# Performance work log

Measured on AMD Instinct MI355X. Metric: run time of the kernel, lower is better.

The kernel has to match this reference:

```python
import jax, jax.numpy as jnp
import numpy as np

SIGMA = 0.5
ALPHA = 1.0  # current_iter = 0 -> cosine annealing returns alpha_max
KSIZE = 5
B, C, H, W, NBOX = 16, 256, 80, 80, 32


def _gaussian_kernel():
    # matches torch: arange(-5//2+1, 5//2+1) = [-2,-1,0,1,2]
    ax = jnp.arange(-(KSIZE // 2), KSIZE // 2 + 1, dtype=jnp.float32)
    xx, yy = jnp.meshgrid(ax, ax, indexing='ij')
    k = jnp.exp(-(xx ** 2 + yy ** 2) / (2.0 * SIGMA ** 2))
    return (k / k.sum())[None, None]  # [1,1,5,5] OIHW


def setup_inputs() -> dict:
    key = jax.random.key(0)
    k1, k2 = jax.random.split(key)
    x = jax.random.normal(k1, (B, C, H, W), dtype=jnp.float32)
    # normalized xywh boxes in [0,1] (code path box.max() <= 1.0)
    boxes = jax.random.uniform(k2, (B, NBOX, 4), dtype=jnp.float32)
    return {"x": x, "boxes": boxes, "kernel": _gaussian_kernel()}


def _attention_map(boxes, height, width):
    # Vectorized rasterization of all boxes at once (torch loops per box).
    xc, yc, bw, bh = boxes[..., 0], boxes[..., 1], boxes[..., 2], boxes[..., 3]
    # int() truncates toward zero -> jnp.trunc; then clamp as in torch code
    x1 = jnp.maximum(0.0, jnp.trunc((xc - bw / 2) * width)).astype(jnp.int32)
    y1 = jnp.maximum(0.0, jnp.trunc((yc - bh / 2) * height)).astype(jnp.int32)
    x2 = jnp.minimum(float(width - 1), jnp.trunc((xc + bw / 2) * width)).astype(jnp.int32)
    y2 = jnp.minimum(float(height - 1), jnp.trunc((yc + bh / 2) * height)).astype(jnp.int32)
    valid = (x2 > x1) & (y2 > y1)  # [B, N]
    rows = jnp.arange(height, dtype=jnp.int32)[None, None, :, None]  # [1,1,H,1]
    cols = jnp.arange(width, dtype=jnp.int32)[None, None, None, :]   # [1,1,1,W]
    inside = ((rows >= y1[:, :, None, None]) & (rows <= y2[:, :, None, None]) &
              (cols >= x1[:, :, None, None]) & (cols <= x2[:, :, None, None]) &
              valid[:, :, None, None])  # [B,N,H,W]
    mask = jnp.any(inside, axis=1).astype(jnp.float32)  # union over boxes -> [B,H,W]
    return mask[:, None]  # [B,1,H,W]


def _smooth(att, kernel):
    pad = KSIZE // 2
    att = jnp.pad(att, ((0, 0), (0, 0), (pad, pad), (pad, pad)), mode='reflect')
    return jax.lax.conv_general_dilated(
        att, kernel, window_strides=(1, 1), padding='VALID',
        dimension_numbers=('NCHW', 'OIHW', 'NCHW'))


def reference(x, boxes, kernel):
    _, _, height, width = x.shape
    att = _attention_map(boxes, height, width)      # [B,1,H,W]
    att = _smooth(att, kernel)                      # gaussian smoothing (sigma>0)
    return x + ALPHA * att * x                      # broadcast over channels
```

## Files before the change

### kernel.cpp

```cpp
#include <hip/hip_runtime.h>


namespace {
constexpr int kB = 16;
constexpr int kC = 256;
constexpr int kH = 80;
constexpr int kW = 80;
constexpr int kNBox = 32;
constexpr float kAlpha = 1.0f;

__device__ __forceinline__ int reflect_idx(int r, int n) {
    return r < 0 ? -r : (r > n - 1 ? 2 * (n - 1) - r : r);
}
}

__global__ __launch_bounds__(320) void ae_fused_kernel(
    const float* __restrict__ x,
    const float* __restrict__ boxes,
    const float* __restrict__ gk,
    float* __restrict__ out)
{
    __shared__ int sx1[kNBox], sy1[kNBox], sx2[kNBox], sy2[kNBox];
    __shared__ float sk[25];
    __shared__ float smask[5][kW];
    __shared__ __attribute__((aligned(16))) float sfac[kW];

    const int b = blockIdx.x / kH;
    const int h = blockIdx.x % kH;
    const int t = threadIdx.x;

    if (t < kNBox) {
        const float* bp = boxes + (size_t)(b * kNBox + t) * 4;
        float xc = bp[0], yc = bp[1], bw = bp[2], bh = bp[3];
        float fx1 = fmaxf(0.0f, truncf((xc - bw * 0.5f) * (float)kW));
        float fy1 = fmaxf(0.0f, truncf((yc - bh * 0.5f) * (float)kH));
        float fx2 = fminf((float)(kW - 1), truncf((xc + bw * 0.5f) * (float)kW));
        float fy2 = fminf((float)(kH - 1), truncf((yc + bh * 0.5f) * (float)kH));
        int ix1 = (int)fx1, iy1 = (int)fy1, ix2 = (int)fx2, iy2 = (int)fy2;
        bool valid = (ix2 > ix1) && (iy2 > iy1);
        sx1[t] = ix1;
        sx2[t] = ix2;
        sy1[t] = valid ? iy1 : 1;
        sy2[t] = valid ? iy2 : 0;
    } else if (t >= 64 && t < 64 + 25) {
        sk[t - 64] = gk[t - 64];
    }
    __syncthreads();

    for (int p = t; p < 5 * kW; p += 320) {
        int i = p / kW, c = p % kW;
        int rr = reflect_idx(h + i - 2, kH);
        float m = 0.0f;
#pragma unroll
        for (int n = 0; n < kNBox; ++n) {
            bool in = (rr >= sy1[n]) && (rr <= sy2[n]) && (c >= sx1[n]) && (c <= sx2[n]);
            m = in ? 1.0f : m;
        }
        smask[i][c] = m;
    }
    __syncthreads();

    if (t < kW) {
        float acc = 0.0f;
#pragma unroll
        for (int i = 0; i < 5; ++i) {
#pragma unroll
            for (int j = 0; j < 5; ++j) {
                int cc = reflect_idx(t + j - 2, kW);
                acc += sk[i * 5 + j] * smask[i][cc];
            }
        }
        sfac[t] = 1.0f + kAlpha * acc;
    }
    __syncthreads();

    const int j = t % 20;
    const int c0 = t / 20;
    const float4 f4 = *reinterpret_cast<const float4*>(&sfac[j * 4]);
    const size_t rowbase = (size_t)b * (kC * kH * kW / 4) + (size_t)h * (kW / 4);
    const float4* x4 = reinterpret_cast<const float4*>(x) + rowbase;
    float4* o4 = reinterpret_cast<float4*>(out) + rowbase;
#pragma unroll
    for (int it = 0; it < kC / 16; ++it) {
        int c = c0 + it * 16;
        size_t off = (size_t)c * (kH * kW / 4) + j;
        float4 v = x4[off];
        v.x *= f4.x;
        v.y *= f4.y;
        v.z *= f4.z;
        v.w *= f4.w;
        o4[off] = v;
    }
}

extern "C" void kernel_launch(void* const* d_in, const int* in_sizes, int n_in,
                              void* d_out, int out_size, void* d_ws, size_t ws_size,
                              hipStream_t stream) {
    const float* x     = (const float*)d_in[0];
    const float* boxes = (const float*)d_in[1];
    const float* gk    = (const float*)d_in[2];
    float* out         = (float*)d_out;

    dim3 grid(kB * kH);
    dim3 block(320);
    ae_fused_kernel<<<grid, block, 0, stream>>>(x, boxes, gk, out);
}
```

Measured before the change: 201.3 us.

## Split into per-batch rasterize kernel and flat streaming multiply kernel

Moves mask rasterization and Gaussian smoothing into a small kernel that runs once per batch and writes a factor map to workspace. A second kernel then streams x with a flat float4 index, multiplying by the precomputed factor, over many more blocks (3200 instead of 1280). This drops the redundant per-row box rasterization and gives the memory-bound pass simpler addressing and more parallelism. The cost is an extra launch, a serial dependency, and a rasterize stage that uses only 16 blocks. If the workspace is too small it falls back to the old fused kernel.

```diff
diff --git a/kernel.cpp b/kernel.cpp
--- a/kernel.cpp
+++ b/kernel.cpp
@@ -8,10 +8,94 @@
 constexpr int kW = 80;
 constexpr int kNBox = 32;
 constexpr float kAlpha = 1.0f;
+constexpr int kHW = kH * kW;
+constexpr int kHW4 = kHW / 4;
+constexpr int kBF4 = kC * kHW4;
+constexpr size_t kWsNeed = (size_t)kB * kHW * sizeof(float);
 
 __device__ __forceinline__ int reflect_idx(int r, int n) {
     return r < 0 ? -r : (r > n - 1 ? 2 * (n - 1) - r : r);
 }
+}
+
+__global__ __launch_bounds__(256) void ae_rasterize_kernel(
+    const float* __restrict__ boxes,
+    const float* __restrict__ gk,
+    float* __restrict__ fac)
+{
+    __shared__ int sx1[kNBox], sy1[kNBox], sx2[kNBox], sy2[kNBox];
+    __shared__ float sk[25];
+    __shared__ float smask[kH][kW];
+
+    const int b = blockIdx.x;
+    const int t = threadIdx.x;
+
+    if (t < kNBox) {
+        const float* bp = boxes + (size_t)(b * kNBox + t) * 4;
+        float xc = bp[0], yc = bp[1], bw = bp[2], bh = bp[3];
+        float fx1 = fmaxf(0.0f, truncf((xc - bw * 0.5f) * (float)kW));
+        float fy1 = fmaxf(0.0f, truncf((yc - bh * 0.5f) * (float)kH));
+        float fx2 = fminf((float)(kW - 1), truncf((xc + bw * 0.5f) * (float)kW));
+        float fy2 = fminf((float)(kH - 1), truncf((yc + bh * 0.5f) * (float)kH));
+        int ix1 = (int)fx1, iy1 = (int)fy1, ix2 = (int)fx2, iy2 = (int)fy2;
+        bool valid = (ix2 > ix1) && (iy2 > iy1);
+        sx1[t] = ix1;
+        sx2[t] = ix2;
+        sy1[t] = valid ? iy1 : 1;
+        sy2[t] = valid ? iy2 : 0;
+    } else if (t >= 64 && t < 64 + 25) {
+        sk[t - 64] = gk[t - 64];
+    }
+    __syncthreads();
+
+    for (int p = t; p < kHW; p += 256) {
+        int h = p / kW, w = p % kW;
+        float m = 0.0f;
+#pragma unroll
+        for (int n = 0; n < kNBox; ++n) {
+            bool in = (h >= sy1[n]) && (h <= sy2[n]) && (w >= sx1[n]) && (w <= sx2[n]);
+            m = in ? 1.0f : m;
+        }
+        smask[h][w] = m;
+    }
+    __syncthreads();
+
+    for (int p = t; p < kHW; p += 256) {
+        int h = p / kW, w = p % kW;
+        float acc = 0.0f;
+#pragma unroll
+        for (int i = 0; i < 5; ++i) {
+            int rr = reflect_idx(h + i - 2, kH);
+#pragma unroll
+            for (int j = 0; j < 5; ++j) {
+                int cc = reflect_idx(w + j - 2, kW);
+                acc += sk[i * 5 + j] * smask[rr][cc];
+            }
+        }
+        fac[(size_t)b * kHW + p] = 1.0f + kAlpha * acc;
+    }
+}
+
+__global__ __launch_bounds__(256) void ae_stream_kernel(
+    const float4* __restrict__ x4,
+    const float4* __restrict__ fac4,
+    float4* __restrict__ o4)
+{
+    const int blk = blockIdx.x;
+    const int b = blk / 200;
+    const int off = (blk % 200) * 256 + threadIdx.x;
+    const float4 f = fac4[b * kHW4 + (off % kHW4)];
+    const size_t base = (size_t)b * kBF4 + off;
+#pragma unroll
+    for (int k = 0; k < 8; ++k) {
+        size_t idx = base + (size_t)k * 51200;
+        float4 v = x4[idx];
+        v.x *= f.x;
+        v.y *= f.y;
+        v.z *= f.z;
+        v.w *= f.w;
+        o4[idx] = v;
+    }
 }
 
 __global__ __launch_bounds__(320) void ae_fused_kernel(
@@ -101,7 +185,12 @@
     const float* gk    = (const float*)d_in[2];
     float* out         = (float*)d_out;
 
-    dim3 grid(kB * kH);
-    dim3 block(320);
-    ae_fused_kernel<<<grid, block, 0, stream>>>(x, boxes, gk, out);
+    if (ws_size >= kWsNeed) {
+        float* fac = (float*)d_ws;
+        ae_rasterize_kernel<<<dim3(kB), dim3(256), 0, stream>>>(boxes, gk, fac);
+        ae_stream_kernel<<<dim3(kB * 200), dim3(256), 0, stream>>>(
+            (const float4*)x, (const float4*)fac, (float4*)out);
+    } else {
+        ae_fused_kernel<<<dim3(kB * kH), dim3(320), 0, stream>>>(x, boxes, gk, out);
+    }
 }
```

Result: slower. 229.1 us (+13.8%).
